# Performance work log

Measured on AMD Instinct MI355X. Metric: run time of the kernel, lower is better.

## Reference

```python
import jax, jax.numpy as jnp
import numpy as np

B, NP, D, K, H = 2, 512, 768, 64, 8
HD = D // H  # head dim = 96


def layernorm(x, g, b, eps=1e-5):
    m = jnp.mean(x, axis=-1, keepdims=True)
    v = jnp.mean((x - m) ** 2, axis=-1, keepdims=True)
    return (x - m) / jnp.sqrt(v + eps) * g + b


def setup_inputs() -> dict:
    key = jax.random.key(0)
    ks = jax.random.split(key, 16)
    s = 0.02
    return {
        "features": jax.random.normal(ks[0], (B, NP, D), jnp.float32),
        "points_xyz": jax.random.normal(ks[1], (B, NP, 3), jnp.float32),
        # distance_encoder: Linear(1 -> D)
        "Wd": jax.random.normal(ks[2], (D,), jnp.float32) * s,
        "bd": jnp.zeros((D,), jnp.float32),
        # geo_attention: MultiheadAttention(D, H)
        "Wq": jax.random.normal(ks[3], (D, D), jnp.float32) * s,
        "bq": jnp.zeros((D,), jnp.float32),
        "Wk": jax.random.normal(ks[4], (D, D), jnp.float32) * s,
        "bk": jnp.zeros((D,), jnp.float32),
        "Wv": jax.random.normal(ks[5], (D, D), jnp.float32) * s,
        "bv": jnp.zeros((D,), jnp.float32),
        "Wo": jax.random.normal(ks[6], (D, D), jnp.float32) * s,
        "bo": jnp.zeros((D,), jnp.float32),
        # spatial_enhancer: Linear(2D -> D) + LayerNorm + SiLU
        "We": jax.random.normal(ks[7], (2 * D, D), jnp.float32) * s,
        "be": jnp.zeros((D,), jnp.float32),
        "g_ln": jnp.ones((D,), jnp.float32),
        "b_ln": jnp.zeros((D,), jnp.float32),
    }


def reference(features, points_xyz, Wd, bd, Wq, bq, Wk, bk, Wv, bv, Wo, bo, We, be, g_ln, b_ln):
    # pairwise distances per batch: [B, Np, Np]
    sq = jnp.sum(points_xyz ** 2, axis=-1)
    d2 = sq[:, :, None] + sq[:, None, :] - 2.0 * jnp.einsum("bnd,bmd->bnm", points_xyz, points_xyz)
    dist = jnp.sqrt(jnp.maximum(d2, 0.0))
    # k nearest neighbors (smallest distances)
    neg_d, idx = jax.lax.top_k(-dist, K)          # idx: [B, Np, K]
    nbr_dist = -neg_d                              # [B, Np, K]
    # gather neighbor features: [B, Np, K, D]
    nbr_feat = jax.vmap(lambda f, i: f[i])(features, idx)
    # distance encoder: Linear(1->D) on unsqueezed distances
    dist_feat = nbr_dist[..., None] * Wd + bd      # [B, Np, K, D]
    kv = nbr_feat + dist_feat
    # multi-head attention: per-point query over its K neighbors
    q = (features @ Wq + bq).reshape(B, NP, H, HD)
    k = (kv @ Wk + bk).reshape(B, NP, K, H, HD)
    v = (kv @ Wv + bv).reshape(B, NP, K, H, HD)
    scores = jnp.einsum("bnhd,bnkhd->bnhk", q, k) / jnp.sqrt(jnp.float32(HD))
    attn = jax.nn.softmax(scores, axis=-1)
    o = jnp.einsum("bnhk,bnkhd->bnhd", attn, v).reshape(B, NP, D)
    attended = o @ Wo + bo                          # [B, Np, D]
    # spatial enhancer on [features ; attended]
    ctx = jnp.concatenate([features, attended], axis=-1)
    enhanced = jax.nn.silu(layernorm(ctx @ We + be, g_ln, b_ln))
    return enhanced
```

## Files before the change

kernel.cpp:

```cpp
#include <hip/hip_runtime.h>
#include <math.h>

#define NPTS 512
#define DIM  768
#define KNN  64
#define NH   8
#define HDIM 96
#define MROWS 1024
#define MPAD  1088
#define WOROWS 832
#define WSQ   ((size_t)DIM * DIM)

typedef unsigned short u16;
typedef unsigned long long ull;
typedef __attribute__((ext_vector_type(8))) short short8;
typedef __attribute__((ext_vector_type(4))) float f32x4;

__device__ __forceinline__ unsigned f2bf(float f) {
    unsigned u = __float_as_uint(f);
    return (u + 0x7fffu + ((u >> 16) & 1u)) >> 16;
}
__device__ __forceinline__ float bf2f(u16 v) {
    return __uint_as_float(((unsigned)v) << 16);
}
__device__ __forceinline__ void gload_lds16(const void* g, void* l) {
    __builtin_amdgcn_global_load_lds(
        (const __attribute__((address_space(1))) void*)g,
        (__attribute__((address_space(3))) void*)l, 16, 0, 0);
}
__device__ __forceinline__ ull shfl_xor_u64(ull x, int j) {
    unsigned lo = (unsigned)x, hi = (unsigned)(x >> 32);
    lo = __shfl_xor(lo, j); hi = __shfl_xor(hi, j);
    return ((ull)hi << 32) | lo;
}
__device__ __forceinline__ ull merge_discard(ull a, ull b, int lane, bool clean) {
    ull rev = shfl_xor_u64(b, 63);
    ull m = a < rev ? a : rev;
    if (clean) {
#pragma unroll
        for (int j = 32; j > 0; j >>= 1) {
            ull p = shfl_xor_u64(m, j);
            bool keep_lo = ((lane & j) == 0);
            bool alt = m < p;
            ull lo = alt ? m : p, hi = alt ? p : m;
            m = keep_lo ? lo : hi;
        }
    }
    return m;
}

__global__ __launch_bounds__(256) void mega_prep_k(
    const float* __restrict__ features,
    const float* __restrict__ Wd, const float* __restrict__ bd,
    const float* __restrict__ Wq, const float* __restrict__ Wk, const float* __restrict__ Wv,
    const float* __restrict__ Wo, const float* __restrict__ bo, const float* __restrict__ We,
    u16* __restrict__ Fb, u16* __restrict__ Wob, u16* __restrict__ W3)
{
    __shared__ float T[64][65];
    int bid = blockIdx.x, tid = threadIdx.x;

    if (bid < 768) {
        int i = (bid * 256 + tid) * 4;
        float4 v = *(const float4*)&features[i];
        uint2 o;
        o.x = f2bf(v.x) | (f2bf(v.y) << 16);
        o.y = f2bf(v.z) | (f2bf(v.w) << 16);
        *(uint2*)&Fb[i] = o;
        return;
    }
    if (bid < 816) {
        int flat = (bid - 768) * 1024 + tid * 4;
        int r = flat / DIM, c = flat - r * DIM;
        uint2 o; o.x = 0u; o.y = 0u;
        if (r == 0) {
            float4 v = *(const float4*)&Wd[c];
            o.x = f2bf(v.x) | (f2bf(v.y) << 16);
            o.y = f2bf(v.z) | (f2bf(v.w) << 16);
        } else if (r == 1) {
            float4 v = *(const float4*)&bd[c];
            o.x = f2bf(v.x) | (f2bf(v.y) << 16);
            o.y = f2bf(v.z) | (f2bf(v.w) << 16);
        }
        *(uint2*)&Fb[(size_t)(MROWS + r) * DIM + c] = o;
        return;
    }
    if (bid < 1440) {
        int flat = (bid - 816) * 1024 + tid * 4;
        int r = flat / DIM, c = flat - r * DIM;
        uint2 o; o.x = 0u; o.y = 0u;
        if (r < DIM) {
            float4 v = *(const float4*)&Wo[(size_t)r * DIM + c];
            o.x = f2bf(v.x) | (f2bf(v.y) << 16);
            o.y = f2bf(v.z) | (f2bf(v.w) << 16);
        } else if (r == DIM) {
            float4 v = *(const float4*)&bo[c];
            o.x = f2bf(v.x) | (f2bf(v.y) << 16);
            o.y = f2bf(v.z) | (f2bf(v.w) << 16);
        }
        *(uint2*)&Wob[(size_t)r * DIM + c] = o;
        return;
    }
    {
        int t = bid - 1440;
        int m = t / 144, r2 = t % 144;
        int by = r2 / 12, bx = r2 % 12;
        const float* S = (m == 0) ? Wq : (m == 1) ? Wk : (m == 2) ? Wv
                       : (m == 3) ? We : (We + WSQ);
        u16* D = W3 + (size_t)m * WSQ;
        int r0 = by * 64, c0 = bx * 64;
#pragma unroll
        for (int i = 0; i < 16; ++i) {
            int lin = tid + i * 256;
            int r = lin >> 6, c = lin & 63;
            T[r][c] = S[(size_t)(r0 + r) * DIM + c0 + c];
        }
        __syncthreads();
#pragma unroll
        for (int i = 0; i < 16; ++i) {
            int lin = tid + i * 256;
            int c = lin >> 6, r = lin & 63;
            D[(size_t)(c0 + c) * DIM + r0 + r] = (u16)f2bf(T[r][c]);
        }
    }
}

union alignas(16) GTSm {
    struct { short As[64 * 64]; short Bs[64 * 64]; } g;
    float P[NPTS * 3];
};

__global__ __launch_bounds__(256) void qkvw_topk_k(
    const u16* __restrict__ Fb, const u16* __restrict__ Wob, const u16* __restrict__ W3,
    const float* __restrict__ bq, const float* __restrict__ be,
    const float* __restrict__ pts,
    float* __restrict__ FQ, u16* __restrict__ FKb, u16* __restrict__ FVb,
    u16* __restrict__ WeffT, float* __restrict__ c_e, float* __restrict__ Z0,
    int* __restrict__ idxb, float* __restrict__ distb)
{
    __shared__ GTSm sm;
    int bid = blockIdx.x, tid = threadIdx.x;
    int wv = tid >> 6, lane = tid & 63;

    if (bid < 256) {
        int bn = bid * 4 + wv;
        int b  = bn >> 9;
        int n  = bn & (NPTS - 1);
        const float* pb = pts + (size_t)b * NPTS * 3;
        for (int i = tid; i < NPTS * 3; i += 256) sm.P[i] = pb[i];
        __syncthreads();

        float xn = sm.P[n * 3], yn = sm.P[n * 3 + 1], zn = sm.P[n * 3 + 2];
        float sqn = xn * xn + yn * yn + zn * zn;
        ull key[8];
#pragma unroll
        for (int r = 0; r < 8; ++r) {
            int m = r * 64 + lane;
            float xm = sm.P[m * 3], ym = sm.P[m * 3 + 1], zm = sm.P[m * 3 + 2];
            float d2 = sqn + (xm * xm + ym * ym + zm * zm)
                     - 2.0f * (xn * xm + yn * ym + zn * zm);
            unsigned db = __float_as_uint(fmaxf(d2, 0.0f));
            key[r] = ((ull)db << 32) | (unsigned)m;
        }

#pragma unroll
        for (int k = 2; k <= 64; k <<= 1) {
#pragma unroll
            for (int j = k >> 1; j > 0; j >>= 1) {
#pragma unroll
                for (int r = 0; r < 8; ++r) {
                    ull p = shfl_xor_u64(key[r], j);
                    bool up = ((lane & k) == 0);
                    bool keep_lo = up == ((lane & j) == 0);
                    bool alt = key[r] < p;
                    ull lo = alt ? key[r] : p, hi = alt ? p : key[r];
                    key[r] = keep_lo ? lo : hi;
                }
            }
        }

        key[0] = merge_discard(key[0], key[4], lane, true);
        key[1] = merge_discard(key[1], key[5], lane, true);
        key[2] = merge_discard(key[2], key[6], lane, true);
        key[3] = merge_discard(key[3], key[7], lane, true);
        key[0] = merge_discard(key[0], key[2], lane, true);
        key[1] = merge_discard(key[1], key[3], lane, true);
        key[0] = merge_discard(key[0], key[1], lane, false);

        ull k0 = key[0];
        idxb[(size_t)bn * KNN + lane]  = (int)(k0 & 0xffffffffu);
        distb[(size_t)bn * KNN + lane] = sqrtf(__uint_as_float((unsigned)(k0 >> 32)));
        return;
    }

    int bid2 = bid - 256;
    int z, by, bx;
    if (bid2 < 816) {
        z = bid2 / 204;
        int rem = bid2 - z * 204;
        by = rem / 12; bx = rem - by * 12;
        if (z == 0 && by >= 16) return;
        if (z == 3 && by >= 13) return;
    } else {
        z = 4;
        int rem = bid2 - 816;
        by = rem / 12; bx = rem - by * 12;
    }
    const u16* A  = (z == 3) ? Wob : Fb;
    const u16* BT = W3 + (size_t)((z == 3) ? 4 : (z == 4) ? 3 : z) * WSQ;

    int wr = (wv >> 1) * 32, wc = (wv & 1) * 32;
    int l15 = lane & 15, kg = lane >> 4;
    int brow = by * 64, bcol = bx * 64;

    f32x4 acc[2][2] = {};

    int srow = tid >> 3;
    int sc0  = tid & 7;

    for (int k0 = 0; k0 < DIM; k0 += 64) {
#pragma unroll
        for (int i = 0; i < 2; ++i) {
            int row = srow + i * 32;
            int cs = sc0 ^ (row & 7);
            gload_lds16(&A[(size_t)(brow + row) * DIM + k0 + cs * 8],
                        &sm.g.As[(i * 256 + wv * 64) * 8]);
            gload_lds16(&BT[(size_t)(bcol + row) * DIM + k0 + cs * 8],
                        &sm.g.Bs[(i * 256 + wv * 64) * 8]);
        }
        __syncthreads();
#pragma unroll
        for (int kk = 0; kk < 2; ++kk) {
            int r0 = wr + l15, r1 = wr + 16 + l15;
            int c0 = wc + l15, c1 = wc + 16 + l15;
            short8 a0 = *(const short8*)&sm.g.As[r0 * 64 + ((kk * 4 + kg) ^ (r0 & 7)) * 8];
            short8 a1 = *(const short8*)&sm.g.As[r1 * 64 + ((kk * 4 + kg) ^ (r1 & 7)) * 8];
            short8 b0 = *(const short8*)&sm.g.Bs[c0 * 64 + ((kk * 4 + kg) ^ (c0 & 7)) * 8];
            short8 b1 = *(const short8*)&sm.g.Bs[c1 * 64 + ((kk * 4 + kg) ^ (c1 & 7)) * 8];
            acc[0][0] = __builtin_amdgcn_mfma_f32_16x16x32_bf16(a0, b0, acc[0][0], 0, 0, 0);
            acc[0][1] = __builtin_amdgcn_mfma_f32_16x16x32_bf16(a0, b1, acc[0][1], 0, 0, 0);
            acc[1][0] = __builtin_amdgcn_mfma_f32_16x16x32_bf16(a1, b0, acc[1][0], 0, 0, 0);
            acc[1][1] = __builtin_amdgcn_mfma_f32_16x16x32_bf16(a1, b1, acc[1][1], 0, 0, 0);
        }
        __syncthreads();
    }

#pragma unroll
    for (int m = 0; m < 2; ++m) {
#pragma unroll
        for (int n = 0; n < 2; ++n) {
            int col  = bcol + wc + n * 16 + l15;
            int row0 = brow + wr + m * 16 + kg * 4;
            if (z == 0) {
                float bv = bq[col];
#pragma unroll
                for (int j = 0; j < 4; ++j)
                    FQ[(size_t)(row0 + j) * DIM + col] = acc[m][n][j] + bv;
            } else if (z == 1) {
#pragma unroll
                for (int j = 0; j < 4; ++j)
                    FKb[(size_t)(row0 + j) * DIM + col] = (u16)f2bf(acc[m][n][j]);
            } else if (z == 2) {
#pragma unroll
                for (int j = 0; j < 4; ++j)
                    FVb[(size_t)(row0 + j) * DIM + col] = (u16)f2bf(acc[m][n][j]);
            } else if (z == 4) {
                float bv = be[col];
#pragma unroll
                for (int j = 0; j < 4; ++j)
                    Z0[(size_t)(row0 + j) * DIM + col] = acc[m][n][j] + bv;
            } else {
                if (row0 + 3 < DIM) {
                    ull pk =
                          (ull)f2bf(acc[m][n][0])
                        | ((ull)f2bf(acc[m][n][1]) << 16)
                        | ((ull)f2bf(acc[m][n][2]) << 32)
                        | ((ull)f2bf(acc[m][n][3]) << 48);
                    *(ull*)&WeffT[(size_t)col * DIM + row0] = pk;
                } else {
#pragma unroll
                    for (int j = 0; j < 4; ++j) {
                        int row = row0 + j;
                        if (row < DIM)       WeffT[(size_t)col * DIM + row] = (u16)f2bf(acc[m][n][j]);
                        else if (row == DIM) c_e[col] = acc[m][n][j];
                    }
                }
            }
        }
    }
}

__global__ __launch_bounds__(256) void gemm_z1_k(
    const u16* __restrict__ Ob, const u16* __restrict__ WeffT,
    const float* __restrict__ c_e, float* __restrict__ Z1)
{
    __shared__ short As[64 * 64];
    __shared__ short Bs[64 * 64];

    int tid  = threadIdx.x;
    int wv = tid >> 6, lane = tid & 63;
    int wr = (wv >> 1) * 32, wc = (wv & 1) * 32;
    int l15 = lane & 15, kg = lane >> 4;
    int brow = blockIdx.y * 64, bcol = blockIdx.x * 64;

    f32x4 acc[2][2] = {};

    int srow = tid >> 3;
    int sc0  = tid & 7;

    for (int k0 = 0; k0 < DIM; k0 += 64) {
#pragma unroll
        for (int i = 0; i < 2; ++i) {
            int row = srow + i * 32;
            int cs = sc0 ^ (row & 7);
            gload_lds16(&Ob[(size_t)(brow + row) * DIM + k0 + cs * 8],
                        &As[(i * 256 + wv * 64) * 8]);
            gload_lds16(&WeffT[(size_t)(bcol + row) * DIM + k0 + cs * 8],
                        &Bs[(i * 256 + wv * 64) * 8]);
        }
        __syncthreads();
#pragma unroll
        for (int kk = 0; kk < 2; ++kk) {
            int r0 = wr + l15, r1 = wr + 16 + l15;
            int c0 = wc + l15, c1 = wc + 16 + l15;
            short8 a0 = *(const short8*)&As[r0 * 64 + ((kk * 4 + kg) ^ (r0 & 7)) * 8];
            short8 a1 = *(const short8*)&As[r1 * 64 + ((kk * 4 + kg) ^ (r1 & 7)) * 8];
            short8 b0 = *(const short8*)&Bs[c0 * 64 + ((kk * 4 + kg) ^ (c0 & 7)) * 8];
            short8 b1 = *(const short8*)&Bs[c1 * 64 + ((kk * 4 + kg) ^ (c1 & 7)) * 8];
            acc[0][0] = __builtin_amdgcn_mfma_f32_16x16x32_bf16(a0, b0, acc[0][0], 0, 0, 0);
            acc[0][1] = __builtin_amdgcn_mfma_f32_16x16x32_bf16(a0, b1, acc[0][1], 0, 0, 0);
            acc[1][0] = __builtin_amdgcn_mfma_f32_16x16x32_bf16(a1, b0, acc[1][0], 0, 0, 0);
            acc[1][1] = __builtin_amdgcn_mfma_f32_16x16x32_bf16(a1, b1, acc[1][1], 0, 0, 0);
        }
        __syncthreads();
    }

#pragma unroll
    for (int m = 0; m < 2; ++m) {
#pragma unroll
        for (int n = 0; n < 2; ++n) {
            int col = bcol + wc + n * 16 + l15;
            float bv = c_e[col];
#pragma unroll
            for (int j = 0; j < 4; ++j) {
                int row = brow + wr + m * 16 + kg * 4 + j;
                Z1[(size_t)row * DIM + col] = acc[m][n][j] + bv;
            }
        }
    }
}

__global__ __launch_bounds__(512) void attn_k(
    const float* __restrict__ FQ, const u16* __restrict__ FKb, const u16* __restrict__ FVb,
    const int* __restrict__ idxb, const float* __restrict__ distb,
    const float* __restrict__ bk, const float* __restrict__ bv,
    u16* __restrict__ O)
{
    int bn = blockIdx.x;
    int b  = bn >> 9;
    int tid = threadIdx.x;
    int wv = tid >> 6, lane = tid & 63;

    __shared__ float qlds[NH][104];
    __shared__ int   s_idx[KNN];
    __shared__ float s_dist[KNN];
    __shared__ float s_sc[NH][68];
    __shared__ float s_att[NH][68];
    __shared__ float s_qh[NH][2];
    __shared__ float s_sd[NH];

    if (tid < KNN) {
        s_idx[tid]  = idxb[(size_t)bn * KNN + tid];
        s_dist[tid] = distb[(size_t)bn * KNN + tid];
    }
    const float* qrow = FQ + (size_t)bn * DIM;
    {
        int d = tid;
        if (d < DIM) qlds[d / HDIM][d % HDIM] = qrow[d];
        int d2 = tid + 512;
        if (d2 < DIM) qlds[d2 / HDIM][d2 % HDIM] = qrow[d2];
    }
    __syncthreads();

    {
        int h = wv;
        const u16* wdk = FKb + (size_t)MROWS * DIM + h * HDIM;
        const u16* ckr = FKb + (size_t)(MROWS + 1) * DIM + h * HDIM;
        const float* bkh = bk + h * HDIM;
        float q = qlds[h][lane];
        float pw = q * bf2f(wdk[lane]);
        float pc = q * (bf2f(ckr[lane]) + bkh[lane]);
        if (lane < HDIM - 64) {
            float q2 = qlds[h][lane + 64];
            pw = fmaf(q2, bf2f(wdk[lane + 64]), pw);
            pc = fmaf(q2, bf2f(ckr[lane + 64]) + bkh[lane + 64], pc);
        }
#pragma unroll
        for (int off = 32; off; off >>= 1) {
            pw += __shfl_xor(pw, off);
            pc += __shfl_xor(pc, off);
        }
        if (lane == 0) { s_qh[h][0] = pw; s_qh[h][1] = pc; }
    }

    {
        int j = tid >> 3, h = tid & 7;
        const u16* kr = FKb + (size_t)(b * NPTS + s_idx[j]) * DIM + h * HDIM;
        const uint4* kr4 = (const uint4*)kr;
        float a0 = 0.f, a1 = 0.f, a2 = 0.f, a3 = 0.f;
#pragma unroll
        for (int i = 0; i < 12; ++i) {
            uint4 kv = kr4[i];
            float4 qa = *(const float4*)&qlds[h][i * 8];
            float4 qb = *(const float4*)&qlds[h][i * 8 + 4];
            a0 = fmaf(qa.x, __uint_as_float(kv.x << 16), a0);
            a1 = fmaf(qa.y, __uint_as_float(kv.x & 0xffff0000u), a1);
            a2 = fmaf(qa.z, __uint_as_float(kv.y << 16), a2);
            a3 = fmaf(qa.w, __uint_as_float(kv.y & 0xffff0000u), a3);
            a0 = fmaf(qb.x, __uint_as_float(kv.z << 16), a0);
            a1 = fmaf(qb.y, __uint_as_float(kv.z & 0xffff0000u), a1);
            a2 = fmaf(qb.z, __uint_as_float(kv.w << 16), a2);
            a3 = fmaf(qb.w, __uint_as_float(kv.w & 0xffff0000u), a3);
        }
        s_sc[h][j] = (a0 + a1) + (a2 + a3);
    }
    __syncthreads();

    {
        int h = wv, j = lane;
        const float invs = 0.10206207261596575f;
        float qwdk = s_qh[h][0], qck = s_qh[h][1];
        float dj = s_dist[j];
        float sc = (s_sc[h][j] + dj * qwdk + qck) * invs;
        float mx = sc;
#pragma unroll
        for (int off = 32; off; off >>= 1) mx = fmaxf(mx, __shfl_xor(mx, off));
        float ev = __expf(sc - mx);
        float sum = ev;
#pragma unroll
        for (int off = 32; off; off >>= 1) sum += __shfl_xor(sum, off);
        float att = ev / sum;
        s_att[h][j] = att;
        float sd = att * dj;
#pragma unroll
        for (int off = 32; off; off >>= 1) sd += __shfl_xor(sd, off);
        if (lane == 0) s_sd[h] = sd;
    }
    __syncthreads();

    if (tid < 384) {
        int d0 = tid * 2;
        int h  = d0 / HDIM;
        const float* attp = s_att[h];
        const size_t basev = (size_t)(b * NPTS) * DIM + d0;
        float o0 = 0.f, o1 = 0.f;
#pragma unroll 4
        for (int j = 0; j < KNN; ++j) {
            unsigned pv = *(const unsigned*)&FVb[basev + (size_t)s_idx[j] * DIM];
            float a = attp[j];
            o0 = fmaf(a, __uint_as_float(pv << 16), o0);
            o1 = fmaf(a, __uint_as_float(pv & 0xffff0000u), o1);
        }
        const u16* wdv = FVb + (size_t)MROWS * DIM;
        const u16* cvr = FVb + (size_t)(MROWS + 1) * DIM;
        float sdh = s_sd[h];
        o0 += sdh * bf2f(wdv[d0])     + (bf2f(cvr[d0])     + bv[d0]);
        o1 += sdh * bf2f(wdv[d0 + 1]) + (bf2f(cvr[d0 + 1]) + bv[d0 + 1]);
        unsigned po = f2bf(o0) | (f2bf(o1) << 16);
        *(unsigned*)&O[(size_t)bn * DIM + d0] = po;
    }
}

__global__ __launch_bounds__(192) void ln_silu_k(
    const float* __restrict__ Z0, const float* __restrict__ Z1,
    const float* __restrict__ g, const float* __restrict__ bta,
    float* __restrict__ out)
{
    int bn = blockIdx.x, tid = threadIdx.x;
    size_t ro = (size_t)bn * DIM;
    int e0 = tid * 4;
    float4 x = *(const float4*)&Z0[ro + e0];
    {
        float4 p = *(const float4*)&Z1[ro + e0];
        x.x += p.x; x.y += p.y; x.z += p.z; x.w += p.w;
    }
    float s  = (x.x + x.y) + (x.z + x.w);
    float ss = (x.x * x.x + x.y * x.y) + (x.z * x.z + x.w * x.w);
    __shared__ float red[3][2];
#pragma unroll
    for (int off = 32; off; off >>= 1) {
        s  += __shfl_xor(s, off);
        ss += __shfl_xor(ss, off);
    }
    int w = tid >> 6;
    if ((tid & 63) == 0) { red[w][0] = s; red[w][1] = ss; }
    __syncthreads();
    s  = red[0][0] + red[1][0] + red[2][0];
    ss = red[0][1] + red[1][1] + red[2][1];
    float mean = s * (1.0f / DIM);
    float var  = ss * (1.0f / DIM) - mean * mean;
    float rstd = rsqrtf(var + 1e-5f);
    float4 gv = *(const float4*)&g[e0];
    float4 bv = *(const float4*)&bta[e0];
    float4 y;
    y.x = (x.x - mean) * rstd * gv.x + bv.x;
    y.y = (x.y - mean) * rstd * gv.y + bv.y;
    y.z = (x.z - mean) * rstd * gv.z + bv.z;
    y.w = (x.w - mean) * rstd * gv.w + bv.w;
    float4 o;
    o.x = y.x / (1.0f + __expf(-y.x));
    o.y = y.y / (1.0f + __expf(-y.y));
    o.z = y.z / (1.0f + __expf(-y.z));
    o.w = y.w / (1.0f + __expf(-y.w));
    *(float4*)&out[ro + e0] = o;
}

extern "C" void kernel_launch(void* const* d_in, const int* in_sizes, int n_in,
                              void* d_out, int out_size, void* d_ws, size_t ws_size,
                              hipStream_t stream)
{
    const float* features = (const float*)d_in[0];
    const float* pts      = (const float*)d_in[1];
    const float* Wd       = (const float*)d_in[2];
    const float* bd       = (const float*)d_in[3];
    const float* Wq       = (const float*)d_in[4];
    const float* bq       = (const float*)d_in[5];
    const float* Wk       = (const float*)d_in[6];
    const float* bk       = (const float*)d_in[7];
    const float* Wv       = (const float*)d_in[8];
    const float* bv       = (const float*)d_in[9];
    const float* Wo       = (const float*)d_in[10];
    const float* bo       = (const float*)d_in[11];
    const float* We       = (const float*)d_in[12];
    const float* be       = (const float*)d_in[13];
    const float* g_ln     = (const float*)d_in[14];
    const float* b_ln     = (const float*)d_in[15];

    const size_t MAT  = (size_t)MROWS * DIM;
    const size_t MATP = (size_t)MPAD  * DIM;

    float* ws = (float*)d_ws;
    float* FQ    = ws;
    u16*   FKb   = (u16*)(ws + MATP);
    u16*   FVb   = FKb + MATP;
    u16*   Fb    = FVb + MATP;
    u16*   Ob    = Fb + MATP;
    u16*   Wob   = Ob + MAT;
    u16*   W3    = Wob + (size_t)WOROWS * DIM;
    u16*   WeffT = W3 + 5 * WSQ;
    float* c_e   = (float*)(WeffT + WSQ);
    int*   idxb  = (int*)(c_e + DIM);
    float* distb = (float*)(idxb + (size_t)MROWS * KNN);
    float* Z0    = distb + (size_t)MROWS * KNN;
    float* Z1    = Z0 + MAT;

    mega_prep_k<<<2160, 256, 0, stream>>>(features, Wd, bd, Wq, Wk, Wv, Wo, bo, We,
                                          Fb, Wob, W3);
    qkvw_topk_k<<<1264, 256, 0, stream>>>(
        Fb, Wob, W3, bq, be, pts, FQ, FKb, FVb, WeffT, c_e, Z0, idxb, distb);
    attn_k<<<MROWS, 512, 0, stream>>>(FQ, FKb, FVb, idxb, distb, bk, bv, Ob);
    gemm_z1_k<<<dim3(12, 16), 256, 0, stream>>>(Ob, WeffT, c_e, Z1);
    ln_silu_k<<<MROWS, 192, 0, stream>>>(Z0, Z1, g_ln, b_ln, (float*)d_out);
}
```

Baseline: 67.77 us.

## Replace register shuffle top-k with shared-memory bitonic sort on packed 32-bit keys

Result: slower. 85.55 us (+26.2%).

```diff
diff --git a/kernel.cpp b/kernel.cpp
--- a/kernel.cpp
+++ b/kernel.cpp
@@ -27,26 +27,6 @@
     __builtin_amdgcn_global_load_lds(
         (const __attribute__((address_space(1))) void*)g,
         (__attribute__((address_space(3))) void*)l, 16, 0, 0);
-}
-__device__ __forceinline__ ull shfl_xor_u64(ull x, int j) {
-    unsigned lo = (unsigned)x, hi = (unsigned)(x >> 32);
-    lo = __shfl_xor(lo, j); hi = __shfl_xor(hi, j);
-    return ((ull)hi << 32) | lo;
-}
-__device__ __forceinline__ ull merge_discard(ull a, ull b, int lane, bool clean) {
-    ull rev = shfl_xor_u64(b, 63);
-    ull m = a < rev ? a : rev;
-    if (clean) {
-#pragma unroll
-        for (int j = 32; j > 0; j >>= 1) {
-            ull p = shfl_xor_u64(m, j);
-            bool keep_lo = ((lane & j) == 0);
-            bool alt = m < p;
-            ull lo = alt ? m : p, hi = alt ? p : m;
-            m = keep_lo ? lo : hi;
-        }
-    }
-    return m;
 }
 
 __global__ __launch_bounds__(256) void mega_prep_k(
@@ -126,7 +106,7 @@
 
 union alignas(16) GTSm {
     struct { short As[64 * 64]; short Bs[64 * 64]; } g;
-    float P[NPTS * 3];
+    struct { float P[NPTS * 3]; unsigned keys[4][NPTS]; } tk;
 };
 
 __global__ __launch_bounds__(256) void qkvw_topk_k(
@@ -142,53 +122,54 @@
     int wv = tid >> 6, lane = tid & 63;
 
     if (bid < 256) {
-        int bn = bid * 4 + wv;
+        int sub = wv;
+        int bn = bid * 4 + sub;
         int b  = bn >> 9;
         int n  = bn & (NPTS - 1);
         const float* pb = pts + (size_t)b * NPTS * 3;
-        for (int i = tid; i < NPTS * 3; i += 256) sm.P[i] = pb[i];
-        __syncthreads();
-
-        float xn = sm.P[n * 3], yn = sm.P[n * 3 + 1], zn = sm.P[n * 3 + 2];
+        for (int i = tid; i < NPTS * 3; i += 256) sm.tk.P[i] = pb[i];
+        __syncthreads();
+
+        float xn = sm.tk.P[n * 3], yn = sm.tk.P[n * 3 + 1], zn = sm.tk.P[n * 3 + 2];
         float sqn = xn * xn + yn * yn + zn * zn;
-        ull key[8];
+        unsigned kreg[8];
 #pragma unroll
         for (int r = 0; r < 8; ++r) {
             int m = r * 64 + lane;
-            float xm = sm.P[m * 3], ym = sm.P[m * 3 + 1], zm = sm.P[m * 3 + 2];
+            float xm = sm.tk.P[m * 3], ym = sm.tk.P[m * 3 + 1], zm = sm.tk.P[m * 3 + 2];
             float d2 = sqn + (xm * xm + ym * ym + zm * zm)
                      - 2.0f * (xn * xm + yn * ym + zn * zm);
             unsigned db = __float_as_uint(fmaxf(d2, 0.0f));
-            key[r] = ((ull)db << 32) | (unsigned)m;
-        }
-
-#pragma unroll
-        for (int k = 2; k <= 64; k <<= 1) {
-#pragma unroll
+            kreg[r] = (db & 0xFFFFFE00u) | (unsigned)m;
+        }
+        __syncthreads();
+        unsigned* keys = sm.tk.keys[sub];
+#pragma unroll
+        for (int r = 0; r < 8; ++r) keys[r * 64 + lane] = kreg[r];
+        __syncthreads();
+
+        for (int k = 2; k <= NPTS; k <<= 1) {
             for (int j = k >> 1; j > 0; j >>= 1) {
 #pragma unroll
                 for (int r = 0; r < 8; ++r) {
-                    ull p = shfl_xor_u64(key[r], j);
-                    bool up = ((lane & k) == 0);
-                    bool keep_lo = up == ((lane & j) == 0);
-                    bool alt = key[r] < p;
-                    ull lo = alt ? key[r] : p, hi = alt ? p : key[r];
-                    key[r] = keep_lo ? lo : hi;
+                    int i = r * 64 + lane;
+                    int ixj = i ^ j;
+                    if (ixj > i) {
+                        bool asc = ((i & k) == 0);
+                        unsigned a = keys[i], bb = keys[ixj];
+                        if ((a > bb) == asc) { keys[i] = bb; keys[ixj] = a; }
+                    }
                 }
+                __syncthreads();
             }
         }
 
-        key[0] = merge_discard(key[0], key[4], lane, true);
-        key[1] = merge_discard(key[1], key[5], lane, true);
-        key[2] = merge_discard(key[2], key[6], lane, true);
-        key[3] = merge_discard(key[3], key[7], lane, true);
-        key[0] = merge_discard(key[0], key[2], lane, true);
-        key[1] = merge_discard(key[1], key[3], lane, true);
-        key[0] = merge_discard(key[0], key[1], lane, false);
-
-        ull k0 = key[0];
-        idxb[(size_t)bn * KNN + lane]  = (int)(k0 & 0xffffffffu);
-        distb[(size_t)bn * KNN + lane] = sqrtf(__uint_as_float((unsigned)(k0 >> 32)));
+        if (lane == tid - sub * 64 && lane < 64) {  }
+        {
+            unsigned kk = keys[lane];
+            idxb[(size_t)bn * KNN + lane]  = (int)(kk & 511u);
+            distb[(size_t)bn * KNN + lane] = sqrtf(__uint_as_float(kk & 0xFFFFFE00u));
+        }
         return;
     }
 
```

## Split per-point top-k across four waves with shared-memory merge

Applied to the files above, without the earlier changes.

Result: no change. 68.28 us (+0.8%).

```diff
diff --git a/kernel.cpp b/kernel.cpp
--- a/kernel.cpp
+++ b/kernel.cpp
@@ -126,7 +126,7 @@
 
 union alignas(16) GTSm {
     struct { short As[64 * 64]; short Bs[64 * 64]; } g;
-    float P[NPTS * 3];
+    struct { float P[NPTS * 3]; ull L[4][64]; } tk;
 };
 
 __global__ __launch_bounds__(256) void qkvw_topk_k(
@@ -141,21 +141,21 @@
     int bid = blockIdx.x, tid = threadIdx.x;
     int wv = tid >> 6, lane = tid & 63;
 
-    if (bid < 256) {
-        int bn = bid * 4 + wv;
+    if (bid < 1024) {
+        int bn = bid;
         int b  = bn >> 9;
         int n  = bn & (NPTS - 1);
         const float* pb = pts + (size_t)b * NPTS * 3;
-        for (int i = tid; i < NPTS * 3; i += 256) sm.P[i] = pb[i];
-        __syncthreads();
-
-        float xn = sm.P[n * 3], yn = sm.P[n * 3 + 1], zn = sm.P[n * 3 + 2];
+        for (int i = tid; i < NPTS * 3; i += 256) sm.tk.P[i] = pb[i];
+        __syncthreads();
+
+        float xn = sm.tk.P[n * 3], yn = sm.tk.P[n * 3 + 1], zn = sm.tk.P[n * 3 + 2];
         float sqn = xn * xn + yn * yn + zn * zn;
-        ull key[8];
-#pragma unroll
-        for (int r = 0; r < 8; ++r) {
-            int m = r * 64 + lane;
-            float xm = sm.P[m * 3], ym = sm.P[m * 3 + 1], zm = sm.P[m * 3 + 2];
+        ull key[2];
+#pragma unroll
+        for (int r = 0; r < 2; ++r) {
+            int m = wv * 128 + r * 64 + lane;
+            float xm = sm.tk.P[m * 3], ym = sm.tk.P[m * 3 + 1], zm = sm.tk.P[m * 3 + 2];
             float d2 = sqn + (xm * xm + ym * ym + zm * zm)
                      - 2.0f * (xn * xm + yn * ym + zn * zm);
             unsigned db = __float_as_uint(fmaxf(d2, 0.0f));
@@ -167,7 +167,7 @@
 #pragma unroll
             for (int j = k >> 1; j > 0; j >>= 1) {
 #pragma unroll
-                for (int r = 0; r < 8; ++r) {
+                for (int r = 0; r < 2; ++r) {
                     ull p = shfl_xor_u64(key[r], j);
                     bool up = ((lane & k) == 0);
                     bool keep_lo = up == ((lane & j) == 0);
@@ -178,21 +178,24 @@
             }
         }
 
-        key[0] = merge_discard(key[0], key[4], lane, true);
-        key[1] = merge_discard(key[1], key[5], lane, true);
-        key[2] = merge_discard(key[2], key[6], lane, true);
-        key[3] = merge_discard(key[3], key[7], lane, true);
-        key[0] = merge_discard(key[0], key[2], lane, true);
-        key[1] = merge_discard(key[1], key[3], lane, true);
-        key[0] = merge_discard(key[0], key[1], lane, false);
-
-        ull k0 = key[0];
-        idxb[(size_t)bn * KNN + lane]  = (int)(k0 & 0xffffffffu);
-        distb[(size_t)bn * KNN + lane] = sqrtf(__uint_as_float((unsigned)(k0 >> 32)));
+        ull w64 = merge_discard(key[0], key[1], lane, true);
+        sm.tk.L[wv][lane] = w64;
+        __syncthreads();
+
+        ull l0 = sm.tk.L[0][lane], l1 = sm.tk.L[1][lane];
+        ull l2 = sm.tk.L[2][lane], l3 = sm.tk.L[3][lane];
+        ull m01 = merge_discard(l0, l1, lane, true);
+        ull m23 = merge_discard(l2, l3, lane, true);
+        ull fin = merge_discard(m01, m23, lane, false);
+
+        if (wv == 0) {
+            idxb[(size_t)bn * KNN + lane]  = (int)(fin & 0xffffffffu);
+            distb[(size_t)bn * KNN + lane] = sqrtf(__uint_as_float((unsigned)(fin >> 32)));
+        }
         return;
     }
 
-    int bid2 = bid - 256;
+    int bid2 = bid - 1024;
     int z, by, bx;
     if (bid2 < 816) {
         z = bid2 / 204;
@@ -555,7 +558,7 @@
 
     mega_prep_k<<<2160, 256, 0, stream>>>(features, Wd, bd, Wq, Wk, Wv, Wo, bo, We,
                                           Fb, Wob, W3);
-    qkvw_topk_k<<<1264, 256, 0, stream>>>(
+    qkvw_topk_k<<<2032, 256, 0, stream>>>(
         Fb, Wob, W3, bq, be, pts, FQ, FKb, FVb, WeffT, c_e, Z0, idxb, distb);
     attn_k<<<MROWS, 512, 0, stream>>>(FQ, FKb, FVb, idxb, distb, bk, bv, Ob);
     gemm_z1_k<<<dim3(12, 16), 256, 0, stream>>>(Ob, WeffT, c_e, Z1);
```
